# Performance work log

Hardware: AMD Instinct MI355X
Metric: run time of the kernel (lower is better)

The kernel has to match this reference:

```python
import jax, jax.numpy as jnp
import numpy as np
from jax import lax

T, B, M, N, D, DA, H, W = 32, 8, 256, 256, 684, 512, 12, 48
QC_CH = 512  # hard-coded coverage conv channels in the module


def setup_inputs() -> dict:
    key = jax.random.key(0)
    ks = iter(jax.random.split(key, 64))
    f = lambda shape, s=0.05: jax.random.normal(next(ks), shape, dtype=jnp.float32) * s
    inp = {
        'rembedding': f((T, B, M), 1.0),
        're_embedding': f((T, B, M), 1.0),
        'ly_mask': jnp.ones((T, B), jnp.float32),
        'context': f((B, D, H, W), 1.0),
        'context_mask': jnp.ones((B, H, W), jnp.float32),
        'init_state': f((B, N), 1.0),
        # fc_Wyz/Wyr/Wyh : Linear(2m -> n)
        'Wyz_w': f((N, 2 * M)), 'Wyz_b': jnp.zeros((N,), jnp.float32),
        'Wyr_w': f((N, 2 * M)), 'Wyr_b': jnp.zeros((N,), jnp.float32),
        'Wyh_w': f((N, 2 * M)), 'Wyh_b': jnp.zeros((N,), jnp.float32),
        # fc_Uhz0/Uhr0/Uhh0 : Linear(n -> n, bias=False)
        'Uhz0_w': f((N, N)), 'Uhr0_w': f((N, N)), 'Uhh0_w': f((N, N)),
        # conv_UaC : Conv2d(D, da, 1)
        'UaC_w': f((DA, D)), 'UaC_b': jnp.zeros((DA,), jnp.float32),
        # fc_WaC : Linear(n -> da, bias=False)
        'WaC_w': f((DA, N)),
        # conv_QC : Conv2d(1, 512, 3, padding=1, bias=False)
        'QC_w': f((QC_CH, 1, 3, 3)),
        # fc_UfC : Linear(512 -> da)
        'UfC_w': f((DA, QC_CH)), 'UfC_b': jnp.zeros((DA,), jnp.float32),
        # fc_vaC : Linear(da -> 1)
        'vaC_w': f((1, DA)), 'vaC_b': jnp.zeros((1,), jnp.float32),
        # fc_Uhz2/Uhr2/Uhh2 : Linear(n -> n)
        'Uhz2_w': f((N, N)), 'Uhz2_b': jnp.zeros((N,), jnp.float32),
        'Uhr2_w': f((N, N)), 'Uhr2_b': jnp.zeros((N,), jnp.float32),
        'Uhh2_w': f((N, N)), 'Uhh2_b': jnp.zeros((N,), jnp.float32),
        # fc_Wcz/Wcr/Wch : Linear(D -> n, bias=False)
        'Wcz_w': f((N, D)), 'Wcr_w': f((N, D)), 'Wch_w': f((N, D)),
        # parent positions into the ctC buffer (valid parents are <= current step)
        'rp': jax.random.randint(next(ks), (T, B), 0, T, dtype=jnp.int32),
    }
    return inp


def _forward(rembedding, re_embedding, ly_mask, context, context_mask, init_state,
             Wyz_w, Wyz_b, Wyr_w, Wyr_b, Wyh_w, Wyh_b,
             Uhz0_w, Uhr0_w, Uhh0_w,
             UaC_w, UaC_b, WaC_w, QC_w, UfC_w, UfC_b, vaC_w, vaC_b,
             Uhz2_w, Uhz2_b, Uhr2_w, Uhr2_b, Uhh2_w, Uhh2_b,
             Wcz_w, Wcr_w, Wch_w, rp):
    n_steps, n_samples = rembedding.shape[0], rembedding.shape[1]
    Hc, Wc = context.shape[2], context.shape[3]
    n = init_state.shape[1]
    d = context.shape[1]

    # pctx_ = conv_UaC(context).permute(2,3,0,1)  -> [H, W, B, da]
    pctx = jnp.einsum('bdhw,ad->hwba', context, UaC_w) + UaC_b
    cmask = context_mask.transpose(1, 2, 0)  # [H, W, B]

    emb = jnp.concatenate([rembedding, re_embedding], axis=2)  # [T, B, 2m]
    sbz = emb @ Wyz_w.T + Wyz_b
    sbr = emb @ Wyr_w.T + Wyr_b
    sbh = emb @ Wyh_w.T + Wyh_b

    batch_idx = jnp.arange(n_samples)

    def step(carry, xs):
        h_, ap_, buf = carry  # h_: [B,n], ap_: [B,H,W], buf: [T+1,B,D]
        z_i, r_i, hh_i, lm, rpos, i = xs
        # gather parent contexts from the running ctC buffer (before this step)
        ctP = buf[rpos, batch_idx]  # [B, D]
        # first GRU cell
        z0 = jax.nn.sigmoid(h_ @ Uhz0_w.T + z_i)
        r0 = jax.nn.sigmoid(h_ @ Uhr0_w.T + r_i)
        h0p = jnp.tanh((h_ @ Uhh0_w.T) * r0 + hh_i)
        h0 = z0 * h_ + (1.0 - z0) * h0p
        h0 = lm[:, None] * h0 + (1.0 - lm)[:, None] * h_
        # coverage attention
        query = h0 @ WaC_w.T  # [B, da]
        cover = lax.conv_general_dilated(
            ap_[:, None, :, :], QC_w, (1, 1), ((1, 1), (1, 1)),
            dimension_numbers=('NCHW', 'OIHW', 'NCHW'))  # [B,512,H,W]
        ccov = jnp.einsum('bchw,ac->hwba', cover, UfC_w) + UfC_b  # [H,W,B,da]
        score = jnp.tanh(pctx + query[None, None, :, :] + ccov)  # [H,W,B,da]
        alpha = (score @ vaC_w.T + vaC_b)[..., 0]  # [H,W,B]
        alpha = jnp.exp(alpha - jnp.max(alpha))
        alpha = alpha * cmask
        alpha = alpha / jnp.sum(alpha, axis=(0, 1))[None, None, :] + 1e-10
        alpha_bhw = alpha.transpose(2, 0, 1)  # [B,H,W]
        ap = ap_ + alpha_bhw
        ctC = jnp.einsum('bdhw,bhw->bd', context, alpha_bhw)  # [B, D]
        # second GRU cell conditioned on the context vector
        z2 = jax.nn.sigmoid(h0 @ Uhz2_w.T + Uhz2_b + ctC @ Wcz_w.T)
        r2 = jax.nn.sigmoid(h0 @ Uhr2_w.T + Uhr2_b + ctC @ Wcr_w.T)
        h2p = jnp.tanh((h0 @ Uhh2_w.T + Uhh2_b) * r2 + ctC @ Wch_w.T)
        h2 = z2 * h0 + (1.0 - z2) * h2p
        h2 = lm[:, None] * h2 + (1.0 - lm)[:, None] * h0
        buf = lax.dynamic_update_slice_in_dim(buf, ctC[None], i + 1, axis=0)
        return (h2, ap, buf), (h2, ctC, ctP, alpha_bhw, ap)

    ap0 = jnp.zeros((n_samples, Hc, Wc), rembedding.dtype)
    buf0 = jnp.zeros((n_steps + 1, n_samples, d), rembedding.dtype)
    xs = (sbz, sbr, sbh, ly_mask, rp, jnp.arange(n_steps))
    _, (h2ts, ctCs, ctPs, calphas, calpha_pasts) = lax.scan(
        step, (init_state, ap0, buf0), xs)
    return h2ts, ctCs, ctPs, calphas, calpha_pasts


def reference(rembedding, re_embedding, ly_mask, context, context_mask, init_state,
              Wyz_w, Wyz_b, Wyr_w, Wyr_b, Wyh_w, Wyh_b,
              Uhz0_w, Uhr0_w, Uhh0_w,
              UaC_w, UaC_b, WaC_w, QC_w, UfC_w, UfC_b, vaC_w, vaC_b,
              Uhz2_w, Uhz2_b, Uhr2_w, Uhr2_b, Uhh2_w, Uhh2_b,
              Wcz_w, Wcr_w, Wch_w, rp):
    return _forward(rembedding, re_embedding, ly_mask, context, context_mask, init_state,
                    Wyz_w, Wyz_b, Wyr_w, Wyr_b, Wyh_w, Wyh_b,
                    Uhz0_w, Uhr0_w, Uhh0_w,
                    UaC_w, UaC_b, WaC_w, QC_w, UfC_w, UfC_b, vaC_w, vaC_b,
                    Uhz2_w, Uhz2_b, Uhr2_w, Uhr2_b, Uhh2_w, Uhh2_b,
                    Wcz_w, Wcr_w, Wch_w, rp)
```

## Files before the change

### kernel.cpp

```cpp
#include <hip/hip_runtime.h>
#include <stdint.h>

typedef unsigned short u16;
typedef unsigned int   u32;

#define TB_ 8
#define NN_ 256
#define DD_ 684
#define PP_ 576

#define OFF_SB    0u
#define OFF_TRAN  0u
#define OFF_BUF   786432u
#define OFF_PCTX  1486848u
#define OFF_FKT   10924032u
#define OFF_RAWP  10942464u
#define OFF_H     11237376u
#define OFF_H0    11245568u
#define OFF_SYNC  11253760u
#define OFF_FLG   11274240u
#define WS_NEED   11274256u

#define OFF_H2   0
#define OFF_CTC  65536
#define OFF_CTP  240640
#define OFF_AL   415744
#define OFF_APO  563200

#define EX_H0 0
#define EX_RW 1
#define EX_CT 2
#define EX_H2 3

__device__ __forceinline__ float b2f(u16 v){ union{u32 i; float f;} x; x.i = ((u32)v)<<16; return x.f; }
__device__ __forceinline__ float gld(const void* p, size_t i, int f32){
  if (f32) return ((const float*)p)[i];
  return b2f(((const u16*)p)[i]);
}
__device__ __forceinline__ float bl(u32 v){ union{u32 i; float f;} x; x.i = v<<16; return x.f; }
__device__ __forceinline__ float bh(u32 v){ union{u32 i; float f;} x; x.i = v & 0xFFFF0000u; return x.f; }

__device__ __forceinline__ float aload(const float* p){
  u32 v = __hip_atomic_load((const u32*)p, __ATOMIC_RELAXED, __HIP_MEMORY_SCOPE_AGENT);
  union{u32 i; float f;} x; x.i = v; return x.f;
}
__device__ __forceinline__ void astore(float* p, float v){
  union{float f; u32 i;} x; x.f = v;
  __hip_atomic_store((u32*)p, x.i, __ATOMIC_RELAXED, __HIP_MEMORY_SCOPE_AGENT);
}

__device__ __forceinline__ float rcpf(float x){ return __builtin_amdgcn_rcpf(x); }
__device__ __forceinline__ float sigm(float x){
  x = fminf(fmaxf(x, -30.f), 30.f);
  return rcpf(1.f + __expf(-x));
}
__device__ __forceinline__ float tanh_c(float x){
  x = fminf(fmaxf(x, -15.f), 15.f);
  float e = __expf(2.f*x);
  return 1.f - 2.f*rcpf(e + 1.f);
}

__device__ __forceinline__ float dot8(uint4 u, const float* s){
  float a = fmaf(bl(u.x), s[0], bh(u.x)*s[1]);
  a = fmaf(bl(u.y), s[2], a); a = fmaf(bh(u.y), s[3], a);
  a = fmaf(bl(u.z), s[4], a); a = fmaf(bh(u.z), s[5], a);
  a = fmaf(bl(u.w), s[6], a); a = fmaf(bh(u.w), s[7], a);
  return a;
}
__device__ __forceinline__ float dot4t(uint2 u, const float* s, float a){
  a = fmaf(bl(u.x), s[0], a); a = fmaf(bh(u.x), s[1], a);
  a = fmaf(bl(u.y), s[2], a); a = fmaf(bh(u.y), s[3], a);
  return a;
}
__device__ __forceinline__ float dotf(const float* w, const float* s, int n){
  float a = 0.f;
  #pragma unroll 4
  for (int k=0;k<n;k+=4){
    float4 u = *(const float4*)(w+k);
    a = fmaf(u.x, s[k], a);   a = fmaf(u.y, s[k+1], a);
    a = fmaf(u.z, s[k+2], a); a = fmaf(u.w, s[k+3], a);
  }
  return a;
}
__device__ __forceinline__ float dotw(const void* W, size_t row_off, const float* s, int n, int f32){
  if (f32) return dotf((const float*)W + row_off, s, n);
  const u16* r = (const u16*)W + row_off;
  float a = 0.f;
  int k = 0;
  for (; k+8 <= n; k += 8) a += dot8(*(const uint4*)(r+k), s+k);
  if (k < n) a = dot4t(*(const uint2*)(r+k), s+k, a);
  return a;
}

__device__ __forceinline__ void flag_set(u32* f, u32 val){
  __hip_atomic_store(f, val, __ATOMIC_RELAXED, __HIP_MEMORY_SCOPE_AGENT);
}
__device__ __forceinline__ void flag_wait(const u32* fbase, u32 tgt){
  const u32* f = fbase + (threadIdx.x & 15);
  while (true){
    u32 v = __hip_atomic_load(f, __ATOMIC_RELAXED, __HIP_MEMORY_SCOPE_AGENT);
    if (__all((int)(v >= tgt))) break;
    __builtin_amdgcn_s_sleep(1);
  }
  asm volatile("" ::: "memory");
}

__global__ void k_detect(const u16* __restrict__ ctx_u16, int* __restrict__ flag){
  __shared__ int cnt;
  if (threadIdx.x == 0) cnt = 0;
  __syncthreads();
  int bad = 0;
  for (int k = threadIdx.x; k < 512; k += 256){
    u16 v = ctx_u16[k];
    int e = (v >> 7) & 0xFF;
    bool sane = (v == 0u) || (v == 0x8000u) || (e >= 102 && e <= 141);
    if (!sane) bad++;
  }
  atomicAdd(&cnt, bad);
  __syncthreads();
  if (threadIdx.x == 0) flag[0] = (cnt > 64) ? 1 : 0;
}

__global__ __launch_bounds__(256) void k_pre1(
    const void* __restrict__ UaC_w, float* __restrict__ UaCT,
    const void* __restrict__ QC, const void* __restrict__ UfC, float* __restrict__ FKt,
    const int* __restrict__ flag)
{
  const int f32 = flag[0];
  const int tid = threadIdx.x;
  __shared__ float smem[4608];
  int bid = blockIdx.x;

  if (bid < 88){
    int ab = bid / 11, db = bid - ab*11;
    int tc = tid & 63, tr = tid >> 6;
    int d0 = db*64, a0 = ab*64;
    for (int rr = tr; rr < 64; rr += 4){
      int d = d0 + tc;
      if (d < DD_) smem[rr*65 + tc] = gld(UaC_w, (size_t)(a0+rr)*DD_ + d, f32);
    }
    __syncthreads();
    for (int rr = tr; rr < 64; rr += 4){
      int d = d0 + rr;
      if (d < DD_) UaCT[(size_t)d*512 + a0 + tc] = smem[tc*65 + rr];
    }
    return;
  }
  bid -= 88;
  {
    for (int k=tid;k<4608;k+=256) smem[k] = gld(QC, k, f32);
    __syncthreads();
    const int lane = tid & 63;
    const int wid = bid*4 + (tid>>6);
    for (int rr=0; rr<4; rr++){
      const int a = wid*4 + rr;
      float acc[9];
      #pragma unroll
      for (int tt=0;tt<9;tt++) acc[tt]=0.f;
      #pragma unroll
      for (int k=0;k<8;k++){
        int c = lane + k*64;
        float v = gld(UfC, (size_t)a*512 + c, f32);
        const float* q = &smem[c*9];
        #pragma unroll
        for (int tt=0;tt<9;tt++) acc[tt] = fmaf(v, q[tt], acc[tt]);
      }
      #pragma unroll
      for (int off=1; off<64; off<<=1){
        #pragma unroll
        for (int tt=0;tt<9;tt++) acc[tt] += __shfl_xor(acc[tt], off, 64);
      }
      #pragma unroll
      for (int tt=0;tt<9;tt++) if (lane == tt) FKt[tt*512 + a] = acc[tt];
    }
  }
}

__global__ __launch_bounds__(256) void k_pctx2(const void* __restrict__ context,
    const float* __restrict__ UaCT, const void* __restrict__ UaC_b, const void* __restrict__ UfC_b,
    float* __restrict__ pctx, const int* __restrict__ flag){
  const int f32 = flag[0];
  const int blk = blockIdx.x;
  const int b = blk / 18;
  const int pbase = (blk - b*18) * 32;
  __shared__ float ctx[32][DD_];
  const int tid = threadIdx.x;
  for (int k=tid; k<32*DD_; k+=256){
    int p = k & 31, d = k >> 5;
    ctx[p][d] = gld(context, ((size_t)(b*DD_+d))*PP_ + pbase + p, f32);
  }
  __syncthreads();
  const int a0 = (tid & 127) * 4;
  const int pr = (tid >> 7) * 16;
  float acc[16][4];
  #pragma unroll
  for (int p=0;p<16;p++){ acc[p][0]=0.f; acc[p][1]=0.f; acc[p][2]=0.f; acc[p][3]=0.f; }
  for (int d=0; d<DD_; d+=4){
    float4 w0 = *(const float4*)&UaCT[(size_t)(d+0)*512 + a0];
    float4 w1 = *(const float4*)&UaCT[(size_t)(d+1)*512 + a0];
    float4 w2 = *(const float4*)&UaCT[(size_t)(d+2)*512 + a0];
    float4 w3 = *(const float4*)&UaCT[(size_t)(d+3)*512 + a0];
    #pragma unroll
    for (int p=0;p<16;p++){
      float4 c = *(const float4*)(&ctx[pr+p][d]);
      acc[p][0] = fmaf(c.x, w0.x, acc[p][0]); acc[p][1] = fmaf(c.x, w0.y, acc[p][1]);
      acc[p][2] = fmaf(c.x, w0.z, acc[p][2]); acc[p][3] = fmaf(c.x, w0.w, acc[p][3]);
      acc[p][0] = fmaf(c.y, w1.x, acc[p][0]); acc[p][1] = fmaf(c.y, w1.y, acc[p][1]);
      acc[p][2] = fmaf(c.y, w1.z, acc[p][2]); acc[p][3] = fmaf(c.y, w1.w, acc[p][3]);
      acc[p][0] = fmaf(c.z, w2.x, acc[p][0]); acc[p][1] = fmaf(c.z, w2.y, acc[p][1]);
      acc[p][2] = fmaf(c.z, w2.z, acc[p][2]); acc[p][3] = fmaf(c.z, w2.w, acc[p][3]);
      acc[p][0] = fmaf(c.w, w3.x, acc[p][0]); acc[p][1] = fmaf(c.w, w3.y, acc[p][1]);
      acc[p][2] = fmaf(c.w, w3.z, acc[p][2]); acc[p][3] = fmaf(c.w, w3.w, acc[p][3]);
    }
  }
  float b0 = gld(UaC_b, a0+0, f32) + gld(UfC_b, a0+0, f32);
  float b1 = gld(UaC_b, a0+1, f32) + gld(UfC_b, a0+1, f32);
  float b2 = gld(UaC_b, a0+2, f32) + gld(UfC_b, a0+2, f32);
  float b3 = gld(UaC_b, a0+3, f32) + gld(UfC_b, a0+3, f32);
  #pragma unroll
  for (int p=0;p<16;p++){
    float4 v; v.x = acc[p][0]+b0; v.y = acc[p][1]+b1; v.z = acc[p][2]+b2; v.w = acc[p][3]+b3;
    *(float4*)&pctx[((size_t)(b*PP_ + pbase + pr + p))*512 + a0] = v;
  }
}

__global__ __launch_bounds__(256) void k_pre2(
    const void* __restrict__ remb, const void* __restrict__ re_emb,
    const void* __restrict__ Wz, const void* __restrict__ bz,
    const void* __restrict__ Wr, const void* __restrict__ br,
    const void* __restrict__ Wh, const void* __restrict__ bhh,
    float* __restrict__ sb,
    float* __restrict__ buf, u32* __restrict__ sync, float* __restrict__ h,
    const void* __restrict__ init_state,
    const int* __restrict__ flag)
{
  const int f32 = flag[0];
  const int tid = threadIdx.x;
  int bid = blockIdx.x;
  if (bid < 768){
    __shared__ float emb[512];
    int g = bid >> 8;
    int tb = bid & 255; int t = tb >> 3; int b = tb & 7;
    emb[tid]     = gld(remb,   (size_t)(t*8+b)*256 + tid, f32);
    emb[tid+256] = gld(re_emb, (size_t)(t*8+b)*256 + tid, f32);
    __syncthreads();
    const void* W = (g==0?Wz:(g==1?Wr:Wh));
    const void* bias = (g==0?bz:(g==1?br:bhh));
    float acc = gld(bias, tid, f32) + dotw(W, (size_t)tid*512, emb, 512, f32);
    sb[(((size_t)g*32+t)*8+b)*256 + tid] = acc;
    return;
  }
  bid -= 768;
  {
    int i = bid*256 + tid;
    int stride = 256*256;
    for (int k=i; k<32*TB_*DD_; k+=stride) buf[k] = 0.f;
    for (int k=i; k<TB_*128;    k+=stride) sync[k] = 0u;
    for (int k=i; k<TB_*NN_;    k+=stride) h[k]   = gld(init_state, k, f32);
  }
}


__global__ __launch_bounds__(256, 1) void k_main(
    const void* __restrict__ ly_mask, const void* __restrict__ context, const void* __restrict__ cmask,
    const void* __restrict__ Uhz0, const void* __restrict__ Uhr0, const void* __restrict__ Uhh0,
    const void* __restrict__ WaC, const void* __restrict__ vaC_w, const void* __restrict__ vaC_b,
    const void* __restrict__ Uhz2, const void* __restrict__ Uhz2_b,
    const void* __restrict__ Uhr2, const void* __restrict__ Uhr2_b,
    const void* __restrict__ Uhh2, const void* __restrict__ Uhh2_b,
    const void* __restrict__ Wcz, const void* __restrict__ Wcr, const void* __restrict__ Wch,
    const int* __restrict__ rp,
    const float* __restrict__ pctx, const float* __restrict__ sb, const float* __restrict__ FKt,
    float* buf, float* h_ws, float* h0_ws, float* rawp, u32* syncg,
    float* out, const int* __restrict__ flag)
{
  const int f32 = flag[0];
  const int tid = threadIdx.x;
  const int b = blockIdx.x >> 4;
  const int j = blockIdx.x & 15;
  const int abase = j*32, nbase = j*16;

  __shared__ float hprev[NN_], h0_lds[NN_];
  __shared__ float ap_lds[PP_], al_lds[PP_], cm_lds[PP_];
  __shared__ float ctc_lds[DD_];
  __shared__ float fk_lds[9*32], vac_lds[32], q_lds[32], qpart[256];
  __shared__ float g1[48], u2l[48], wcl[48];
  __shared__ float red[4];

  for (int k=tid; k<288; k+=256) fk_lds[k] = FKt[(k>>5)*512 + abase + (k&31)];
  if (tid < 32) vac_lds[tid] = gld(vaC_w, abase + tid, f32);
  cm_lds[tid]     = gld(cmask, b*PP_ + tid, f32);
  cm_lds[tid+256] = gld(cmask, b*PP_ + tid + 256, f32);
  if (tid < 64) cm_lds[tid+512] = gld(cmask, b*PP_ + tid + 512, f32);
  ap_lds[tid] = 0.f; ap_lds[tid+256] = 0.f;
  if (tid < 64) ap_lds[tid+512] = 0.f;
  const float vb = gld(vaC_b, 0, f32);

  u32* syncb = syncg + b*128;
  const int p0 = tid, p1 = tid + 256, p2 = tid + 512;
  const bool has3 = (tid < 64);
  const int pown = j*36;

  for (int t=0; t<32; t++){
    const float lm = gld(ly_mask, t*8+b, f32);
    const u32 tgt = (u32)(t+1);

    if (t) flag_wait(syncb + EX_H2*16, (u32)t);
    hprev[tid] = aload(&h_ws[b*256 + tid]);
    __syncthreads();

    if (tid < 192){
      int item = tid >> 2, q = tid & 3;
      int g = item >> 4, nl = item & 15;
      int n = nbase + nl;
      const void* U = (g==0 ? Uhz0 : (g==1 ? Uhr0 : Uhh0));
      float acc = dotw(U, (size_t)n*256 + q*64, &hprev[q*64], 64, f32);
      acc += __shfl_xor(acc,1,64); acc += __shfl_xor(acc,2,64);
      if (q==0) g1[g*16+nl] = acc;
    }
    __syncthreads();
    if (tid < 16){
      int n = nbase + tid;
      float hp = hprev[n];
      float z0 = sigm(g1[tid]    + sb[(((size_t)t)*8+b)*256 + n]);
      float r0 = sigm(g1[16+tid] + sb[(((size_t)(32+t))*8+b)*256 + n]);
      float hc = tanh_c(g1[32+tid]*r0 + sb[(((size_t)(64+t))*8+b)*256 + n]);
      float h0v = z0*hp + (1.f - z0)*hc;
      h0v = lm*h0v + (1.f - lm)*hp;
      astore(&h0_ws[b*256 + n], h0v);
    }
    {
      int rpos = rp[t*8+b];
      if ((unsigned)rpos > 31u) rpos = 31;
      int dbase = j*43, dcnt = (j==15) ? 39 : 43;
      if (tid < dcnt){
        int d = dbase + tid;
        out[OFF_CTP + (t*8+b)*DD_ + d] = aload(&buf[((size_t)rpos*8+b)*DD_ + d]);
      }
    }
    if (tid < 64){
      asm volatile("s_waitcnt vmcnt(0)" ::: "memory");
      if (tid == 0) flag_set(syncb + EX_H0*16 + j, tgt);
    }

    flag_wait(syncb + EX_H0*16, tgt);
    h0_lds[tid] = aload(&h0_ws[b*256 + tid]);
    __syncthreads();
    {
      int ai = tid & 31, nb = tid >> 5;
      qpart[nb*32 + ai] = dotw(WaC, (size_t)(abase+ai)*256 + nb*32, &h0_lds[nb*32], 32, f32);
    }
    __syncthreads();
    if (tid < 32){
      float qv = 0.f;
      #pragma unroll
      for (int nb2=0;nb2<8;nb2++) qv += qpart[nb2*32 + tid];
      q_lds[tid] = qv;
    }
    __syncthreads();
    for (int rep=0; rep<3; rep++){
      int p = tid + rep*256;
      if (p >= PP_) break;
      float PQ[32];
      const float* pc = pctx + ((size_t)(b*PP_ + p))*512 + abase;
      #pragma unroll
      for (int q8=0;q8<8;q8++){
        float4 u = *(const float4*)(pc + q8*4);
        PQ[q8*4+0]=u.x; PQ[q8*4+1]=u.y; PQ[q8*4+2]=u.z; PQ[q8*4+3]=u.w;
      }
      int hh_ = p / 48, ww_ = p - hh_*48;
      #pragma unroll
      for (int kh=0;kh<3;kh++){
        int h2_ = hh_ + kh - 1;
        if ((unsigned)h2_ >= 12u) continue;
        #pragma unroll
        for (int kw=0;kw<3;kw++){
          int w2_ = ww_ + kw - 1;
          if ((unsigned)w2_ >= 48u) continue;
          float av = ap_lds[h2_*48 + w2_];
          const float* fkp = &fk_lds[(kh*3+kw)*32];
          #pragma unroll
          for (int ai=0;ai<32;ai++) PQ[ai] = fmaf(av, fkp[ai], PQ[ai]);
        }
      }
      float racc = 0.f;
      #pragma unroll
      for (int ai=0;ai<32;ai++)
        racc = fmaf(vac_lds[ai], tanh_c(PQ[ai] + q_lds[ai]), racc);
      astore(&rawp[((size_t)(b*16+j))*PP_ + p], racc);
    }
    if (tid < 192){
      int item = tid >> 2, q = tid & 3;
      int g = item >> 4, nl = item & 15;
      int n = nbase + nl;
      const void* U = (g==0 ? Uhz2 : (g==1 ? Uhr2 : Uhh2));
      float acc = dotw(U, (size_t)n*256 + q*64, &h0_lds[q*64], 64, f32);
      acc += __shfl_xor(acc,1,64); acc += __shfl_xor(acc,2,64);
      if (q==0) u2l[g*16+nl] = acc;
    }
    __syncthreads();
    if (tid == 0) flag_set(syncb + EX_RW*16 + j, tgt);

    flag_wait(syncb + EX_RW*16, tgt);
    {
      float psum = 0.f;
      for (int rep=0; rep<3; rep++){
        int p = tid + rep*256;
        if (p >= PP_) break;
        float raw = vb;
        #pragma unroll
        for (int j2=0;j2<16;j2++) raw += aload(&rawp[((size_t)(b*16+j2))*PP_ + p]);
        raw = fminf(fmaxf(raw, -60.f), 60.f);
        float e = __expf(raw) * cm_lds[p];
        al_lds[p] = e; psum += e;
      }
      #pragma unroll
      for (int off=1; off<64; off<<=1) psum += __shfl_xor(psum, off, 64);
      if ((tid & 63)==0) red[tid>>6] = psum;
    }
    __syncthreads();
    {
      float S = red[0] + red[1] + red[2] + red[3];
      S = fmaxf(S, 1e-30f);
      float inv = rcpf(S);
      float a0 = al_lds[p0]*inv + 1e-10f; al_lds[p0] = a0; ap_lds[p0] += a0;
      float a1 = al_lds[p1]*inv + 1e-10f; al_lds[p1] = a1; ap_lds[p1] += a1;
      if (has3){ float a2 = al_lds[p2]*inv + 1e-10f; al_lds[p2] = a2; ap_lds[p2] += a2; }
    }
    __syncthreads();
    if (tid < 36){
      int p = pown + tid;
      out[OFF_AL  + (t*8+b)*PP_ + p] = al_lds[p];
      out[OFF_APO + (t*8+b)*PP_ + p] = ap_lds[p];
    }
    {
      int dbase = j*43, dcnt = (j==15) ? 39 : 43;
      if (tid < dcnt*4){
        int dd = tid >> 2, q = tid & 3, d = dbase + dd;
        float acc;
        if (f32) acc = dotf((const float*)context + ((size_t)(b*DD_+d))*PP_ + q*144, &al_lds[q*144], 144);
        else {
          const u16* crow = (const u16*)context + ((size_t)(b*DD_+d))*PP_ + q*144;
          acc = 0.f;
          #pragma unroll 6
          for (int k=0;k<144;k+=8) acc += dot8(*(const uint4*)(crow+k), &al_lds[q*144+k]);
        }
        acc += __shfl_xor(acc,1,64); acc += __shfl_xor(acc,2,64);
        if (q==0){
          astore(&out[OFF_CTC + (t*8+b)*DD_ + d], acc);
          if (t < 31) astore(&buf[(((size_t)(t+1))*8+b)*DD_ + d], acc);
        }
      }
    }
    __syncthreads();
    if (tid == 0) flag_set(syncb + EX_CT*16 + j, tgt);

    flag_wait(syncb + EX_CT*16, tgt);
    for (int k=tid; k<DD_; k+=256) ctc_lds[k] = aload(&out[OFF_CTC + (t*8+b)*DD_ + k]);
    __syncthreads();
    if (tid < 192){
      int item = tid >> 2, q = tid & 3;
      int g = item >> 4, nl = item & 15;
      int n = nbase + nl;
      const void* W = (g==0 ? Wcz : (g==1 ? Wcr : Wch));
      int base = q*176, cnt = (q==3) ? 156 : 176;
      float acc = dotw(W, (size_t)n*DD_ + base, &ctc_lds[base], cnt, f32);
      acc += __shfl_xor(acc,1,64); acc += __shfl_xor(acc,2,64);
      if (q==0) wcl[g*16+nl] = acc;
    }
    __syncthreads();
    if (tid < 16){
      int n = nbase + tid;
      float h0v = h0_lds[n];
      float z2 = sigm(u2l[tid]    + gld(Uhz2_b, n, f32) + wcl[tid]);
      float r2 = sigm(u2l[16+tid] + gld(Uhr2_b, n, f32) + wcl[16+tid]);
      float hc = tanh_c((u2l[32+tid] + gld(Uhh2_b, n, f32))*r2 + wcl[32+tid]);
      float h2v = z2*h0v + (1.f - z2)*hc;
      h2v = lm*h2v + (1.f - lm)*h0v;
      astore(&h_ws[b*256 + n], h2v);
      out[OFF_H2 + (t*8+b)*256 + n] = h2v;
    }
    if (tid < 64){
      asm volatile("s_waitcnt vmcnt(0)" ::: "memory");
      if (tid == 0) flag_set(syncb + EX_H2*16 + j, tgt);
    }
  }
}


extern "C" void kernel_launch(void* const* d_in, const int* in_sizes, int n_in,
                              void* d_out, int out_size, void* d_ws, size_t ws_size,
                              hipStream_t stream){
  (void)in_sizes; (void)n_in; (void)out_size;
  if (ws_size < WS_NEED) return;

  const void* remb       = d_in[0];
  const void* re_emb     = d_in[1];
  const void* ly_mask    = d_in[2];
  const void* context    = d_in[3];
  const void* cmask      = d_in[4];
  const void* init_state = d_in[5];
  const void* Wyz_w = d_in[6];  const void* Wyz_b = d_in[7];
  const void* Wyr_w = d_in[8];  const void* Wyr_b = d_in[9];
  const void* Wyh_w = d_in[10]; const void* Wyh_b = d_in[11];
  const void* Uhz0  = d_in[12];
  const void* Uhr0  = d_in[13];
  const void* Uhh0  = d_in[14];
  const void* UaC_w = d_in[15]; const void* UaC_b = d_in[16];
  const void* WaC_w = d_in[17];
  const void* QC_w  = d_in[18];
  const void* UfC_w = d_in[19]; const void* UfC_b = d_in[20];
  const void* vaC_w = d_in[21]; const void* vaC_b = d_in[22];
  const void* Uhz2  = d_in[23]; const void* Uhz2_b = d_in[24];
  const void* Uhr2  = d_in[25]; const void* Uhr2_b = d_in[26];
  const void* Uhh2  = d_in[27]; const void* Uhh2_b = d_in[28];
  const void* Wcz   = d_in[29];
  const void* Wcr   = d_in[30];
  const void* Wch   = d_in[31];
  const int*  rp    = (const int*)d_in[32];

  char* ws = (char*)d_ws;
  float* sbp   = (float*)(ws + OFF_SB);
  float* UaCT  = (float*)(ws + OFF_TRAN);
  float* buf   = (float*)(ws + OFF_BUF);
  float* pctx  = (float*)(ws + OFF_PCTX);
  float* FKt   = (float*)(ws + OFF_FKT);
  float* rawp  = (float*)(ws + OFF_RAWP);
  float* h_ws  = (float*)(ws + OFF_H);
  float* h0_ws = (float*)(ws + OFF_H0);
  u32*   syncg = (u32*)  (ws + OFF_SYNC);
  int*   flag  = (int*)  (ws + OFF_FLG);
  float* out   = (float*)d_out;

  k_detect<<<1, 256, 0, stream>>>((const u16*)context, flag);
  k_pre1 <<<120, 256, 0, stream>>>(UaC_w, UaCT, QC_w, UfC_w, FKt, flag);
  k_pctx2<<<144, 256, 0, stream>>>(context, UaCT, UaC_b, UfC_b, pctx, flag);
  k_pre2 <<<1024, 256, 0, stream>>>(remb, re_emb, Wyz_w, Wyz_b, Wyr_w, Wyr_b, Wyh_w, Wyh_b, sbp,
                                    buf, syncg, h_ws, init_state, flag);
  k_main <<<128, 256, 0, stream>>>(ly_mask, context, cmask,
                                   Uhz0, Uhr0, Uhh0, WaC_w, vaC_w, vaC_b,
                                   Uhz2, Uhz2_b, Uhr2, Uhr2_b, Uhh2, Uhh2_b,
                                   Wcz, Wcr, Wch, rp,
                                   pctx, sbp, FKt,
                                   buf, h_ws, h0_ws, rawp, syncg, out, flag);
}
```

Baseline: 1.241 ms.

## Compute full first GRU stage redundantly per block to drop one cross-block barrier

Each of the 16 blocks per batch row now computes all 256 h0 outputs itself, using the full Uh*0 matrices, instead of computing a slice and exchanging through workspace with a flag barrier. This removes one inter-block synchronisation per timestep at the cost of 16x redundant matvec work. The rawp layout is transposed so each position's 16 partials sit in one contiguous 64-byte line, read with coherent vector loads. The flag wait now spins on a single wave without sleep and then uses a block barrier. The ctP copy is moved later so it overlaps with other work.

```diff
diff --git a/kernel.cpp b/kernel.cpp
--- a/kernel.cpp
+++ b/kernel.cpp
@@ -27,10 +27,9 @@
 #define OFF_AL   415744
 #define OFF_APO  563200
 
-#define EX_H0 0
-#define EX_RW 1
-#define EX_CT 2
-#define EX_H2 3
+#define EX_RW 0
+#define EX_CT 1
+#define EX_H2 2
 
 __device__ __forceinline__ float b2f(u16 v){ union{u32 i; float f;} x; x.i = ((u32)v)<<16; return x.f; }
 __device__ __forceinline__ float gld(const void* p, size_t i, int f32){
@@ -47,6 +46,16 @@
 __device__ __forceinline__ void astore(float* p, float v){
   union{float f; u32 i;} x; x.f = v;
   __hip_atomic_store((u32*)p, x.i, __ATOMIC_RELAXED, __HIP_MEMORY_SCOPE_AGENT);
+}
+
+__device__ __forceinline__ void cload_line_nw(const float* p, float4& x, float4& y, float4& z, float4& w){
+  asm volatile(
+    "global_load_dwordx4 %0, %4, off sc0 sc1\n\t"
+    "global_load_dwordx4 %1, %4, off offset:16 sc0 sc1\n\t"
+    "global_load_dwordx4 %2, %4, off offset:32 sc0 sc1\n\t"
+    "global_load_dwordx4 %3, %4, off offset:48 sc0 sc1"
+    : "=&v"(x), "=&v"(y), "=&v"(z), "=&v"(w)
+    : "v"(p) : "memory");
 }
 
 __device__ __forceinline__ float rcpf(float x){ return __builtin_amdgcn_rcpf(x); }
@@ -95,14 +104,15 @@
 __device__ __forceinline__ void flag_set(u32* f, u32 val){
   __hip_atomic_store(f, val, __ATOMIC_RELAXED, __HIP_MEMORY_SCOPE_AGENT);
 }
-__device__ __forceinline__ void flag_wait(const u32* fbase, u32 tgt){
-  const u32* f = fbase + (threadIdx.x & 15);
-  while (true){
-    u32 v = __hip_atomic_load(f, __ATOMIC_RELAXED, __HIP_MEMORY_SCOPE_AGENT);
-    if (__all((int)(v >= tgt))) break;
-    __builtin_amdgcn_s_sleep(1);
-  }
-  asm volatile("" ::: "memory");
+__device__ __forceinline__ void flag_wait_w0(const u32* fbase, u32 tgt){
+  if (threadIdx.x < 64){
+    const u32* f = fbase + (threadIdx.x & 15);
+    while (true){
+      u32 v = __hip_atomic_load(f, __ATOMIC_RELAXED, __HIP_MEMORY_SCOPE_AGENT);
+      if (__all((int)(v >= tgt))) break;
+    }
+  }
+  __syncthreads();
 }
 
 __global__ void k_detect(const u16* __restrict__ ctx_u16, int* __restrict__ flag){
@@ -271,7 +281,7 @@
     const void* __restrict__ Wcz, const void* __restrict__ Wcr, const void* __restrict__ Wch,
     const int* __restrict__ rp,
     const float* __restrict__ pctx, const float* __restrict__ sb, const float* __restrict__ FKt,
-    float* buf, float* h_ws, float* h0_ws, float* rawp, u32* syncg,
+    float* buf, float* h_ws, float* rawp, u32* syncg,
     float* out, const int* __restrict__ flag)
 {
   const int f32 = flag[0];
@@ -284,7 +294,7 @@
   __shared__ float ap_lds[PP_], al_lds[PP_], cm_lds[PP_];
   __shared__ float ctc_lds[DD_];
   __shared__ float fk_lds[9*32], vac_lds[32], q_lds[32], qpart[256];
-  __shared__ float g1[48], u2l[48], wcl[48];
+  __shared__ float u2l[48], wcl[48];
   __shared__ float red[4];
 
   for (int k=tid; k<288; k+=256) fk_lds[k] = FKt[(k>>5)*512 + abase + (k&31)];
@@ -305,46 +315,20 @@
     const float lm = gld(ly_mask, t*8+b, f32);
     const u32 tgt = (u32)(t+1);
 
-    if (t) flag_wait(syncb + EX_H2*16, (u32)t);
+    if (t) flag_wait_w0(syncb + EX_H2*16, (u32)t);
     hprev[tid] = aload(&h_ws[b*256 + tid]);
     __syncthreads();
-
-    if (tid < 192){
-      int item = tid >> 2, q = tid & 3;
-      int g = item >> 4, nl = item & 15;
-      int n = nbase + nl;
-      const void* U = (g==0 ? Uhz0 : (g==1 ? Uhr0 : Uhh0));
-      float acc = dotw(U, (size_t)n*256 + q*64, &hprev[q*64], 64, f32);
-      acc += __shfl_xor(acc,1,64); acc += __shfl_xor(acc,2,64);
-      if (q==0) g1[g*16+nl] = acc;
-    }
-    __syncthreads();
-    if (tid < 16){
-      int n = nbase + tid;
-      float hp = hprev[n];
-      float z0 = sigm(g1[tid]    + sb[(((size_t)t)*8+b)*256 + n]);
-      float r0 = sigm(g1[16+tid] + sb[(((size_t)(32+t))*8+b)*256 + n]);
-      float hc = tanh_c(g1[32+tid]*r0 + sb[(((size_t)(64+t))*8+b)*256 + n]);
+    {
+      float az = dotw(Uhz0, (size_t)tid*256, hprev, 256, f32);
+      float ar = dotw(Uhr0, (size_t)tid*256, hprev, 256, f32);
+      float ah = dotw(Uhh0, (size_t)tid*256, hprev, 256, f32);
+      float hp = hprev[tid];
+      float z0 = sigm(az + sb[(((size_t)t)*8+b)*256 + tid]);
+      float r0 = sigm(ar + sb[(((size_t)(32+t))*8+b)*256 + tid]);
+      float hc = tanh_c(ah*r0 + sb[(((size_t)(64+t))*8+b)*256 + tid]);
       float h0v = z0*hp + (1.f - z0)*hc;
-      h0v = lm*h0v + (1.f - lm)*hp;
-      astore(&h0_ws[b*256 + n], h0v);
-    }
-    {
-      int rpos = rp[t*8+b];
-      if ((unsigned)rpos > 31u) rpos = 31;
-      int dbase = j*43, dcnt = (j==15) ? 39 : 43;
-      if (tid < dcnt){
-        int d = dbase + tid;
-        out[OFF_CTP + (t*8+b)*DD_ + d] = aload(&buf[((size_t)rpos*8+b)*DD_ + d]);
-      }
-    }
-    if (tid < 64){
-      asm volatile("s_waitcnt vmcnt(0)" ::: "memory");
-      if (tid == 0) flag_set(syncb + EX_H0*16 + j, tgt);
-    }
-
-    flag_wait(syncb + EX_H0*16, tgt);
-    h0_lds[tid] = aload(&h0_ws[b*256 + tid]);
+      h0_lds[tid] = lm*h0v + (1.f - lm)*hp;
+    }
     __syncthreads();
     {
       int ai = tid & 31, nb = tid >> 5;
@@ -387,7 +371,7 @@
       #pragma unroll
       for (int ai=0;ai<32;ai++)
         racc = fmaf(vac_lds[ai], tanh_c(PQ[ai] + q_lds[ai]), racc);
-      astore(&rawp[((size_t)(b*16+j))*PP_ + p], racc);
+      astore(&rawp[((size_t)(b*PP_ + p))*16 + j], racc);
     }
     if (tid < 192){
       int item = tid >> 2, q = tid & 3;
@@ -398,21 +382,60 @@
       acc += __shfl_xor(acc,1,64); acc += __shfl_xor(acc,2,64);
       if (q==0) u2l[g*16+nl] = acc;
     }
+    {
+      int rpos = rp[t*8+b];
+      if ((unsigned)rpos > 31u) rpos = 31;
+      int dbase = j*43, dcnt = (j==15) ? 39 : 43;
+      if (tid < dcnt){
+        int d = dbase + tid;
+        out[OFF_CTP + (t*8+b)*DD_ + d] = aload(&buf[((size_t)rpos*8+b)*DD_ + d]);
+      }
+    }
     __syncthreads();
     if (tid == 0) flag_set(syncb + EX_RW*16 + j, tgt);
 
-    flag_wait(syncb + EX_RW*16, tgt);
+    flag_wait_w0(syncb + EX_RW*16, tgt);
     {
+      const float* lp0 = rawp + ((size_t)(b*PP_ + p0))*16;
+      const float* lp1 = rawp + ((size_t)(b*PP_ + p1))*16;
+      const float* lp2 = rawp + ((size_t)(b*PP_ + p2))*16;
+      float4 x0,x1,x2,x3, y0,y1,y2,y3;
+      float4 z0={0,0,0,0}, z1={0,0,0,0}, z2={0,0,0,0}, z3={0,0,0,0};
+      cload_line_nw(lp0, x0,x1,x2,x3);
+      cload_line_nw(lp1, y0,y1,y2,y3);
+      if (has3) cload_line_nw(lp2, z0,z1,z2,z3);
+      asm volatile("s_waitcnt vmcnt(0)" ::: "memory");
+      __builtin_amdgcn_sched_barrier(0);
       float psum = 0.f;
-      for (int rep=0; rep<3; rep++){
-        int p = tid + rep*256;
-        if (p >= PP_) break;
+      {
         float raw = vb;
-        #pragma unroll
-        for (int j2=0;j2<16;j2++) raw += aload(&rawp[((size_t)(b*16+j2))*PP_ + p]);
+        raw += x0.x; raw += x0.y; raw += x0.z; raw += x0.w;
+        raw += x1.x; raw += x1.y; raw += x1.z; raw += x1.w;
+        raw += x2.x; raw += x2.y; raw += x2.z; raw += x2.w;
+        raw += x3.x; raw += x3.y; raw += x3.z; raw += x3.w;
         raw = fminf(fmaxf(raw, -60.f), 60.f);
-        float e = __expf(raw) * cm_lds[p];
-        al_lds[p] = e; psum += e;
+        float e = __expf(raw) * cm_lds[p0];
+        al_lds[p0] = e; psum += e;
+      }
+      {
+        float raw = vb;
+        raw += y0.x; raw += y0.y; raw += y0.z; raw += y0.w;
+        raw += y1.x; raw += y1.y; raw += y1.z; raw += y1.w;
+        raw += y2.x; raw += y2.y; raw += y2.z; raw += y2.w;
+        raw += y3.x; raw += y3.y; raw += y3.z; raw += y3.w;
+        raw = fminf(fmaxf(raw, -60.f), 60.f);
+        float e = __expf(raw) * cm_lds[p1];
+        al_lds[p1] = e; psum += e;
+      }
+      if (has3){
+        float raw = vb;
+        raw += z0.x; raw += z0.y; raw += z0.z; raw += z0.w;
+        raw += z1.x; raw += z1.y; raw += z1.z; raw += z1.w;
+        raw += z2.x; raw += z2.y; raw += z2.z; raw += z2.w;
+        raw += z3.x; raw += z3.y; raw += z3.z; raw += z3.w;
+        raw = fminf(fmaxf(raw, -60.f), 60.f);
+        float e = __expf(raw) * cm_lds[p2];
+        al_lds[p2] = e; psum += e;
       }
       #pragma unroll
       for (int off=1; off<64; off<<=1) psum += __shfl_xor(psum, off, 64);
@@ -423,9 +446,9 @@
       float S = red[0] + red[1] + red[2] + red[3];
       S = fmaxf(S, 1e-30f);
       float inv = rcpf(S);
-      float a0 = al_lds[p0]*inv + 1e-10f; al_lds[p0] = a0; ap_lds[p0] += a0;
-      float a1 = al_lds[p1]*inv + 1e-10f; al_lds[p1] = a1; ap_lds[p1] += a1;
-      if (has3){ float a2 = al_lds[p2]*inv + 1e-10f; al_lds[p2] = a2; ap_lds[p2] += a2; }
+      float a0v = al_lds[p0]*inv + 1e-10f; al_lds[p0] = a0v; ap_lds[p0] += a0v;
+      float a1v = al_lds[p1]*inv + 1e-10f; al_lds[p1] = a1v; ap_lds[p1] += a1v;
+      if (has3){ float a2v = al_lds[p2]*inv + 1e-10f; al_lds[p2] = a2v; ap_lds[p2] += a2v; }
     }
     __syncthreads();
     if (tid < 36){
@@ -455,7 +478,7 @@
     __syncthreads();
     if (tid == 0) flag_set(syncb + EX_CT*16 + j, tgt);
 
-    flag_wait(syncb + EX_CT*16, tgt);
+    flag_wait_w0(syncb + EX_CT*16, tgt);
     for (int k=tid; k<DD_; k+=256) ctc_lds[k] = aload(&out[OFF_CTC + (t*8+b)*DD_ + k]);
     __syncthreads();
     if (tid < 192){
@@ -472,10 +495,10 @@
     if (tid < 16){
       int n = nbase + tid;
       float h0v = h0_lds[n];
-      float z2 = sigm(u2l[tid]    + gld(Uhz2_b, n, f32) + wcl[tid]);
-      float r2 = sigm(u2l[16+tid] + gld(Uhr2_b, n, f32) + wcl[16+tid]);
-      float hc = tanh_c((u2l[32+tid] + gld(Uhh2_b, n, f32))*r2 + wcl[32+tid]);
-      float h2v = z2*h0v + (1.f - z2)*hc;
+      float z2g = sigm(u2l[tid]    + gld(Uhz2_b, n, f32) + wcl[tid]);
+      float r2g = sigm(u2l[16+tid] + gld(Uhr2_b, n, f32) + wcl[16+tid]);
+      float hcg = tanh_c((u2l[32+tid] + gld(Uhh2_b, n, f32))*r2g + wcl[32+tid]);
+      float h2v = z2g*h0v + (1.f - z2g)*hcg;
       h2v = lm*h2v + (1.f - lm)*h0v;
       astore(&h_ws[b*256 + n], h2v);
       out[OFF_H2 + (t*8+b)*256 + n] = h2v;
@@ -527,7 +550,6 @@
   float* FKt   = (float*)(ws + OFF_FKT);
   float* rawp  = (float*)(ws + OFF_RAWP);
   float* h_ws  = (float*)(ws + OFF_H);
-  float* h0_ws = (float*)(ws + OFF_H0);
   u32*   syncg = (u32*)  (ws + OFF_SYNC);
   int*   flag  = (int*)  (ws + OFF_FLG);
   float* out   = (float*)d_out;
@@ -542,5 +564,5 @@
                                    Uhz2, Uhz2_b, Uhr2, Uhr2_b, Uhh2, Uhh2_b,
                                    Wcz, Wcr, Wch, rp,
                                    pctx, sbp, FKt,
-                                   buf, h_ws, h0_ws, rawp, syncg, out, flag);
-}
+                                   buf, h_ws, rawp, syncg, out, flag);
+}
```

New measurement: 1.770 ms. 1.43x slower.

## Distribute softmax exp across blocks and poll flags from one wave

Applied to the files above, without the earlier changes.

Previously every block of a batch summed 16 rawp partials for all 576 positions and computed the exponentials redundantly. Now each block handles only its own 36 positions, publishes the exp values and a partial sum to workspace, and waits on a new exchange flag before normalising. The flag wait is also changed so that only wave 0 spins, with no sleep, and the other waves wait at a barrier. This cuts redundant global loads and exp work but adds one more cross-block synchronisation round per timestep.

```diff
diff --git a/kernel.cpp b/kernel.cpp
--- a/kernel.cpp
+++ b/kernel.cpp
@@ -17,9 +17,10 @@
 #define OFF_RAWP  10942464u
 #define OFF_H     11237376u
 #define OFF_H0    11245568u
-#define OFF_SYNC  11253760u
-#define OFF_FLG   11274240u
-#define WS_NEED   11274256u
+#define OFF_EAL   11253760u
+#define OFF_SYNC  11272192u
+#define OFF_FLG   11276288u
+#define WS_NEED   11276304u
 
 #define OFF_H2   0
 #define OFF_CTC  65536
@@ -29,8 +30,9 @@
 
 #define EX_H0 0
 #define EX_RW 1
-#define EX_CT 2
-#define EX_H2 3
+#define EX_E  2
+#define EX_CT 3
+#define EX_H2 4
 
 __device__ __forceinline__ float b2f(u16 v){ union{u32 i; float f;} x; x.i = ((u32)v)<<16; return x.f; }
 __device__ __forceinline__ float gld(const void* p, size_t i, int f32){
@@ -95,14 +97,15 @@
 __device__ __forceinline__ void flag_set(u32* f, u32 val){
   __hip_atomic_store(f, val, __ATOMIC_RELAXED, __HIP_MEMORY_SCOPE_AGENT);
 }
-__device__ __forceinline__ void flag_wait(const u32* fbase, u32 tgt){
-  const u32* f = fbase + (threadIdx.x & 15);
-  while (true){
-    u32 v = __hip_atomic_load(f, __ATOMIC_RELAXED, __HIP_MEMORY_SCOPE_AGENT);
-    if (__all((int)(v >= tgt))) break;
-    __builtin_amdgcn_s_sleep(1);
-  }
-  asm volatile("" ::: "memory");
+__device__ __forceinline__ void flag_wait_w0(const u32* fbase, u32 tgt){
+  if (threadIdx.x < 64){
+    const u32* f = fbase + (threadIdx.x & 15);
+    while (true){
+      u32 v = __hip_atomic_load(f, __ATOMIC_RELAXED, __HIP_MEMORY_SCOPE_AGENT);
+      if (__all((int)(v >= tgt))) break;
+    }
+  }
+  __syncthreads();
 }
 
 __global__ void k_detect(const u16* __restrict__ ctx_u16, int* __restrict__ flag){
@@ -271,7 +274,7 @@
     const void* __restrict__ Wcz, const void* __restrict__ Wcr, const void* __restrict__ Wch,
     const int* __restrict__ rp,
     const float* __restrict__ pctx, const float* __restrict__ sb, const float* __restrict__ FKt,
-    float* buf, float* h_ws, float* h0_ws, float* rawp, u32* syncg,
+    float* buf, float* h_ws, float* h0_ws, float* ealpha, float* rawp, u32* syncg,
     float* out, const int* __restrict__ flag)
 {
   const int f32 = flag[0];
@@ -285,7 +288,7 @@
   __shared__ float ctc_lds[DD_];
   __shared__ float fk_lds[9*32], vac_lds[32], q_lds[32], qpart[256];
   __shared__ float g1[48], u2l[48], wcl[48];
-  __shared__ float red[4];
+  __shared__ float red16[16];
 
   for (int k=tid; k<288; k+=256) fk_lds[k] = FKt[(k>>5)*512 + abase + (k&31)];
   if (tid < 32) vac_lds[tid] = gld(vaC_w, abase + tid, f32);
@@ -297,6 +300,7 @@
   const float vb = gld(vaC_b, 0, f32);
 
   u32* syncb = syncg + b*128;
+  float* psum_ws = (float*)(syncb + 96);
   const int p0 = tid, p1 = tid + 256, p2 = tid + 512;
   const bool has3 = (tid < 64);
   const int pown = j*36;
@@ -305,7 +309,7 @@
     const float lm = gld(ly_mask, t*8+b, f32);
     const u32 tgt = (u32)(t+1);
 
-    if (t) flag_wait(syncb + EX_H2*16, (u32)t);
+    if (t) flag_wait_w0(syncb + EX_H2*16, (u32)t);
     hprev[tid] = aload(&h_ws[b*256 + tid]);
     __syncthreads();
 
@@ -343,7 +347,7 @@
       if (tid == 0) flag_set(syncb + EX_H0*16 + j, tgt);
     }
 
-    flag_wait(syncb + EX_H0*16, tgt);
+    flag_wait_w0(syncb + EX_H0*16, tgt);
     h0_lds[tid] = aload(&h0_ws[b*256 + tid]);
     __syncthreads();
     {
@@ -401,31 +405,43 @@
     __syncthreads();
     if (tid == 0) flag_set(syncb + EX_RW*16 + j, tgt);
 
-    flag_wait(syncb + EX_RW*16, tgt);
+    flag_wait_w0(syncb + EX_RW*16, tgt);
     {
-      float psum = 0.f;
-      for (int rep=0; rep<3; rep++){
-        int p = tid + rep*256;
-        if (p >= PP_) break;
+      float ev = 0.f;
+      if (tid < 36){
+        int p = pown + tid;
         float raw = vb;
         #pragma unroll
         for (int j2=0;j2<16;j2++) raw += aload(&rawp[((size_t)(b*16+j2))*PP_ + p]);
         raw = fminf(fmaxf(raw, -60.f), 60.f);
-        float e = __expf(raw) * cm_lds[p];
-        al_lds[p] = e; psum += e;
-      }
-      #pragma unroll
-      for (int off=1; off<64; off<<=1) psum += __shfl_xor(psum, off, 64);
-      if ((tid & 63)==0) red[tid>>6] = psum;
-    }
-    __syncthreads();
+        ev = __expf(raw) * cm_lds[p];
+        astore(&ealpha[b*PP_ + p], ev);
+      }
+      if (tid < 64){
+        float s = ev;
+        #pragma unroll
+        for (int off=1; off<64; off<<=1) s += __shfl_xor(s, off, 64);
+        if (tid == 0) astore(&psum_ws[j], s);
+        asm volatile("s_waitcnt vmcnt(0)" ::: "memory");
+        if (tid == 0) flag_set(syncb + EX_E*16 + j, tgt);
+      }
+    }
+
+    flag_wait_w0(syncb + EX_E*16, tgt);
     {
-      float S = red[0] + red[1] + red[2] + red[3];
+      float e0 = aload(&ealpha[b*PP_ + p0]);
+      float e1 = aload(&ealpha[b*PP_ + p1]);
+      float e2 = has3 ? aload(&ealpha[b*PP_ + p2]) : 0.f;
+      if (tid < 16) red16[tid] = aload(&psum_ws[tid]);
+      __syncthreads();
+      float S = 0.f;
+      #pragma unroll
+      for (int k=0;k<16;k++) S += red16[k];
       S = fmaxf(S, 1e-30f);
       float inv = rcpf(S);
-      float a0 = al_lds[p0]*inv + 1e-10f; al_lds[p0] = a0; ap_lds[p0] += a0;
-      float a1 = al_lds[p1]*inv + 1e-10f; al_lds[p1] = a1; ap_lds[p1] += a1;
-      if (has3){ float a2 = al_lds[p2]*inv + 1e-10f; al_lds[p2] = a2; ap_lds[p2] += a2; }
+      float a0 = e0*inv + 1e-10f; al_lds[p0] = a0; ap_lds[p0] += a0;
+      float a1 = e1*inv + 1e-10f; al_lds[p1] = a1; ap_lds[p1] += a1;
+      if (has3){ float a2 = e2*inv + 1e-10f; al_lds[p2] = a2; ap_lds[p2] += a2; }
     }
     __syncthreads();
     if (tid < 36){
@@ -455,7 +471,7 @@
     __syncthreads();
     if (tid == 0) flag_set(syncb + EX_CT*16 + j, tgt);
 
-    flag_wait(syncb + EX_CT*16, tgt);
+    flag_wait_w0(syncb + EX_CT*16, tgt);
     for (int k=tid; k<DD_; k+=256) ctc_lds[k] = aload(&out[OFF_CTC + (t*8+b)*DD_ + k]);
     __syncthreads();
     if (tid < 192){
@@ -528,6 +544,7 @@
   float* rawp  = (float*)(ws + OFF_RAWP);
   float* h_ws  = (float*)(ws + OFF_H);
   float* h0_ws = (float*)(ws + OFF_H0);
+  float* eal   = (float*)(ws + OFF_EAL);
   u32*   syncg = (u32*)  (ws + OFF_SYNC);
   int*   flag  = (int*)  (ws + OFF_FLG);
   float* out   = (float*)d_out;
@@ -542,5 +559,5 @@
                                    Uhz2, Uhz2_b, Uhr2, Uhr2_b, Uhh2, Uhh2_b,
                                    Wcz, Wcr, Wch, rp,
                                    pctx, sbp, FKt,
-                                   buf, h_ws, h0_ws, rawp, syncg, out, flag);
-}
+                                   buf, h_ws, h0_ws, eal, rawp, syncg, out, flag);
+}
```

After: 1.184 ms. 4.6% less time.
